# Kernel tuning notes

Measured on AMD Instinct MI355X. Metric: run time of the kernel, lower is better.

The kernel has to match this reference:

```python
import jax, jax.numpy as jnp
import numpy as np

HIDDEN = 1024
SENT = 1024
NS = 8192
NK = 8192


def setup_inputs() -> dict:
    key = jax.random.key(0)
    ks = jax.random.split(key, 6)
    scale = 0.02
    return {
        "sentences_embedding": jax.random.normal(ks[0], (NS, SENT), dtype=jnp.float32),
        "knowledge_embedding": jax.random.normal(ks[1], (NK, 2 * HIDDEN), dtype=jnp.float32),
        "Ws": jax.random.normal(ks[2], (HIDDEN, SENT), dtype=jnp.float32) * scale,
        "bs": jnp.zeros((HIDDEN,), dtype=jnp.float32),
        "Wk": jax.random.normal(ks[3], (HIDDEN, 2 * HIDDEN), dtype=jnp.float32) * scale,
        "bk": jnp.zeros((HIDDEN,), dtype=jnp.float32),
    }


def reference(sentences_embedding, knowledge_embedding, Ws, bs, Wk, bk):
    # S: [Ns, hidden], K: [Nk, hidden] (torch Linear: x @ W.T + b)
    S = sentences_embedding @ Ws.T + bs
    K = knowledge_embedding @ Wk.T + bk
    V = knowledge_embedding  # [Nk, 2*hidden]
    scores = S @ K.T  # [Ns, Nk]
    # NOTE: softmax over dim=0 (across sentences), per the original module
    attns = jax.nn.softmax(scores, axis=0)
    fused_knowledge = attns @ V  # [Ns, 2*hidden]
    return (attns, fused_knowledge)
```

## Files before the change

### kernel.cpp

```cpp
#include <hip/hip_runtime.h>
#include <hip/hip_bf16.h>
#include <math.h>

typedef __bf16 bf16_t;
typedef __bf16 bf16x8 __attribute__((ext_vector_type(8)));
typedef __bf16 bf16x4v __attribute__((ext_vector_type(4)));
typedef float floatx4 __attribute__((ext_vector_type(4)));

#define BM 128
#define BN 128
#define BK 64
#define BK2 128
#define LDT 72

__device__ __forceinline__ void gload_lds16(const void* g, void* l) {
    __builtin_amdgcn_global_load_lds(
        (__attribute__((address_space(1))) void*)g,
        (__attribute__((address_space(3))) void*)l,
        16, 0, 0);
}

__device__ __forceinline__ void split8(const float* p, bf16x8& hi, bf16x8& lo) {
    const float4* q = (const float4*)p;
    float4 a = q[0], b = q[1];
    float v[8] = { a.x, a.y, a.z, a.w, b.x, b.y, b.z, b.w };
#pragma unroll
    for (int i = 0; i < 8; ++i) {
        bf16_t h = (bf16_t)v[i];
        hi[i] = h;
        lo[i] = (bf16_t)(v[i] - (float)h);
    }
}

template<bool OUT_SPLIT, bool HAS_BIAS>
__global__ __launch_bounds__(256, 2)
void gemm_nt_split(const float* __restrict__ A, const float* __restrict__ B,
                   const float* __restrict__ bias,
                   void* __restrict__ C0, bf16_t* __restrict__ Clo,
                   int M, int N, int K)
{
    __shared__ bf16_t Ah[BM * LDT];
    __shared__ bf16_t Al[BM * LDT];
    __shared__ bf16_t Bh[BN * LDT];
    __shared__ bf16_t Bl[BN * LDT];

    const int t    = threadIdx.x;
    const int m0   = blockIdx.x * BM;
    const int n0   = blockIdx.y * BN;
    const int lane = t & 63;
    const int wm   = ((t >> 6) & 1) * 64;
    const int wn   = (t >> 7) * 64;
    const int lr   = lane & 15;
    const int lg   = lane >> 4;

    floatx4 acc[4][4] = {};

    for (int k0 = 0; k0 < K; k0 += BK) {
#pragma unroll
        for (int i = 0; i < 4; ++i) {
            int idx = t + i * 256;
            int row = idx >> 3;
            int col = (idx & 7) << 3;
            bf16x8 h, l;
            split8(&A[(size_t)(m0 + row) * K + k0 + col], h, l);
            *(bf16x8*)&Ah[row * LDT + col] = h;
            *(bf16x8*)&Al[row * LDT + col] = l;
            split8(&B[(size_t)(n0 + row) * K + k0 + col], h, l);
            *(bf16x8*)&Bh[row * LDT + col] = h;
            *(bf16x8*)&Bl[row * LDT + col] = l;
        }
        __syncthreads();
#pragma unroll
        for (int ks = 0; ks < BK; ks += 32) {
            bf16x8 ah[4], al[4], bh[4], bl[4];
#pragma unroll
            for (int mi = 0; mi < 4; ++mi) {
                ah[mi] = *(const bf16x8*)&Ah[(wm + mi * 16 + lr) * LDT + ks + lg * 8];
                al[mi] = *(const bf16x8*)&Al[(wm + mi * 16 + lr) * LDT + ks + lg * 8];
            }
#pragma unroll
            for (int ni = 0; ni < 4; ++ni) {
                bh[ni] = *(const bf16x8*)&Bh[(wn + ni * 16 + lr) * LDT + ks + lg * 8];
                bl[ni] = *(const bf16x8*)&Bl[(wn + ni * 16 + lr) * LDT + ks + lg * 8];
            }
#pragma unroll
            for (int mi = 0; mi < 4; ++mi)
#pragma unroll
                for (int ni = 0; ni < 4; ++ni) {
                    acc[mi][ni] = __builtin_amdgcn_mfma_f32_16x16x32_bf16(ah[mi], bh[ni], acc[mi][ni], 0, 0, 0);
                    acc[mi][ni] = __builtin_amdgcn_mfma_f32_16x16x32_bf16(ah[mi], bl[ni], acc[mi][ni], 0, 0, 0);
                    acc[mi][ni] = __builtin_amdgcn_mfma_f32_16x16x32_bf16(al[mi], bh[ni], acc[mi][ni], 0, 0, 0);
                }
        }
        __syncthreads();
    }

#pragma unroll
    for (int mi = 0; mi < 4; ++mi)
#pragma unroll
        for (int ni = 0; ni < 4; ++ni) {
            int col = n0 + wn + ni * 16 + lr;
            float bv = 0.0f;
            if constexpr (HAS_BIAS) bv = bias[col];
#pragma unroll
            for (int r = 0; r < 4; ++r) {
                int row = m0 + wm + mi * 16 + lg * 4 + r;
                float v = acc[mi][ni][r] + bv;
                if constexpr (OUT_SPLIT) {
                    bf16_t h = (bf16_t)v;
                    ((bf16_t*)C0)[(size_t)row * N + col] = h;
                    Clo[(size_t)row * N + col] = (bf16_t)(v - (float)h);
                } else {
                    ((float*)C0)[(size_t)row * N + col] = v;
                }
            }
        }
}

__global__ __launch_bounds__(256, 2)
void gemm_nt_pre_async(const bf16_t* __restrict__ Ahi, const bf16_t* __restrict__ Alo,
                       const bf16_t* __restrict__ Bhi, const bf16_t* __restrict__ Blo,
                       float* __restrict__ C, float* __restrict__ pm,
                       float* __restrict__ pz, int M, int N, int K)
{
    __shared__ bf16_t Ah[BM * BK];
    __shared__ bf16_t Al[BM * BK];
    __shared__ bf16_t Bh[BN * BK];
    __shared__ bf16_t Bl[BN * BK];
    __shared__ float red_m[2][128];
    __shared__ float red_z[2][128];

    const int t    = threadIdx.x;
    const int m0   = blockIdx.x * BM;
    const int n0   = blockIdx.y * BN;
    const int lane = t & 63;
    const int wv   = t >> 6;
    const int widm = (t >> 6) & 1;
    const int wm   = widm * 64;
    const int wn   = (t >> 7) * 64;
    const int lr   = lane & 15;
    const int lg   = lane >> 4;
    const int lrow = lane >> 3;
    const int lcol = (((lane & 7) ^ lrow) * 8);
    const int swz  = (lr & 7) << 3;

    floatx4 acc[4][4] = {};

    for (int k0 = 0; k0 < K; k0 += BK) {
#pragma unroll
        for (int i = 0; i < 4; ++i) {
            const int seg = wv * 4 + i;
            const int row = seg * 8 + lrow;
            const size_t ga = (size_t)(m0 + row) * K + k0 + lcol;
            const size_t gb = (size_t)(n0 + row) * K + k0 + lcol;
            gload_lds16(&Ahi[ga], &Ah[seg * 512]);
            gload_lds16(&Alo[ga], &Al[seg * 512]);
            gload_lds16(&Bhi[gb], &Bh[seg * 512]);
            gload_lds16(&Blo[gb], &Bl[seg * 512]);
        }
        __syncthreads();
#pragma unroll
        for (int ks = 0; ks < BK; ks += 32) {
            const int cA = (ks + lg * 8) ^ swz;
            bf16x8 ah[4], al[4], bh[4], bl[4];
#pragma unroll
            for (int mi = 0; mi < 4; ++mi) {
                ah[mi] = *(const bf16x8*)&Ah[(wm + mi * 16 + lr) * BK + cA];
                al[mi] = *(const bf16x8*)&Al[(wm + mi * 16 + lr) * BK + cA];
            }
#pragma unroll
            for (int ni = 0; ni < 4; ++ni) {
                bh[ni] = *(const bf16x8*)&Bh[(wn + ni * 16 + lr) * BK + cA];
                bl[ni] = *(const bf16x8*)&Bl[(wn + ni * 16 + lr) * BK + cA];
            }
#pragma unroll
            for (int mi = 0; mi < 4; ++mi)
#pragma unroll
                for (int ni = 0; ni < 4; ++ni) {
                    acc[mi][ni] = __builtin_amdgcn_mfma_f32_16x16x32_bf16(ah[mi], bh[ni], acc[mi][ni], 0, 0, 0);
                    acc[mi][ni] = __builtin_amdgcn_mfma_f32_16x16x32_bf16(ah[mi], bl[ni], acc[mi][ni], 0, 0, 0);
                    acc[mi][ni] = __builtin_amdgcn_mfma_f32_16x16x32_bf16(al[mi], bh[ni], acc[mi][ni], 0, 0, 0);
                }
        }
        __syncthreads();
    }

#pragma unroll
    for (int mi = 0; mi < 4; ++mi)
#pragma unroll
        for (int ni = 0; ni < 4; ++ni) {
            int col = n0 + wn + ni * 16 + lr;
#pragma unroll
            for (int r = 0; r < 4; ++r) {
                int row = m0 + wm + mi * 16 + lg * 4 + r;
                C[(size_t)row * N + col] = acc[mi][ni][r];
            }
        }

#pragma unroll
    for (int ni = 0; ni < 4; ++ni) {
        float lm = -INFINITY;
#pragma unroll
        for (int mi = 0; mi < 4; ++mi)
#pragma unroll
            for (int r = 0; r < 4; ++r) lm = fmaxf(lm, acc[mi][ni][r]);
        float lz = 0.0f;
#pragma unroll
        for (int mi = 0; mi < 4; ++mi)
#pragma unroll
            for (int r = 0; r < 4; ++r) lz += __expf(acc[mi][ni][r] - lm);
#pragma unroll
        for (int off = 16; off <= 32; off <<= 1) {
            float om = __shfl_xor(lm, off);
            float oz = __shfl_xor(lz, off);
            float nm = fmaxf(lm, om);
            lz = lz * __expf(lm - nm) + oz * __expf(om - nm);
            lm = nm;
        }
        if (lg == 0) {
            red_m[widm][wn + ni * 16 + lr] = lm;
            red_z[widm][wn + ni * 16 + lr] = lz;
        }
    }
    __syncthreads();
    if (t < 128) {
        float a = red_m[0][t], b = red_m[1][t];
        float za = red_z[0][t], zb = red_z[1][t];
        float mb = fmaxf(a, b);
        float z  = za * __expf(a - mb) + zb * __expf(b - mb);
        pm[(size_t)blockIdx.x * 8192 + n0 + t] = mb;
        pz[(size_t)blockIdx.x * 8192 + n0 + t] = z;
    }
}

__global__ __launch_bounds__(256, 2)
void gemm_nt_bf16_async(const bf16_t* __restrict__ A, const bf16_t* __restrict__ B,
                        float* __restrict__ C, int M, int N, int K)
{
    __shared__ bf16_t As[BM * BK2];
    __shared__ bf16_t Bs[BN * BK2];

    const int t    = threadIdx.x;
    const int m0   = blockIdx.x * BM;
    const int n0   = blockIdx.y * BN;
    const int lane = t & 63;
    const int wv   = t >> 6;
    const int wm   = ((t >> 6) & 1) * 64;
    const int wn   = (t >> 7) * 64;
    const int lr   = lane & 15;
    const int lg   = lane >> 4;
    const int srow = lane >> 4;
    const int sslt = lane & 15;
    const int swz  = (lr & 7) << 3;

    floatx4 acc[4][4] = {};

    for (int k0 = 0; k0 < K; k0 += BK2) {
#pragma unroll
        for (int i = 0; i < 8; ++i) {
            const int bi  = wv * 8 + i;
            const int row = bi * 4 + srow;
            const int gs  = (sslt & 8) | ((sslt & 7) ^ (row & 7));
            gload_lds16(&A[(size_t)(m0 + row) * K + k0 + gs * 8], &As[bi * 512]);
            gload_lds16(&B[(size_t)(n0 + row) * K + k0 + gs * 8], &Bs[bi * 512]);
        }
        __syncthreads();
#pragma unroll
        for (int ks = 0; ks < BK2; ks += 32) {
            const int cA = (ks + lg * 8) ^ swz;
            bf16x8 a[4], b[4];
#pragma unroll
            for (int mi = 0; mi < 4; ++mi)
                a[mi] = *(const bf16x8*)&As[(wm + mi * 16 + lr) * BK2 + cA];
#pragma unroll
            for (int ni = 0; ni < 4; ++ni)
                b[ni] = *(const bf16x8*)&Bs[(wn + ni * 16 + lr) * BK2 + cA];
#pragma unroll
            for (int mi = 0; mi < 4; ++mi)
#pragma unroll
                for (int ni = 0; ni < 4; ++ni)
                    acc[mi][ni] = __builtin_amdgcn_mfma_f32_16x16x32_bf16(
                        a[mi], b[ni], acc[mi][ni], 0, 0, 0);
        }
        __syncthreads();
    }

#pragma unroll
    for (int mi = 0; mi < 4; ++mi)
#pragma unroll
        for (int ni = 0; ni < 4; ++ni) {
            int col = n0 + wn + ni * 16 + lr;
#pragma unroll
            for (int r = 0; r < 4; ++r) {
                int row = m0 + wm + mi * 16 + lg * 4 + r;
                C[(size_t)row * N + col] = acc[mi][ni][r];
            }
        }
}

__global__ __launch_bounds__(256)
void transpose_to_bf16(const float* __restrict__ src, bf16_t* __restrict__ dst,
                       int R, int Ccols)
{
    __shared__ float tile[64][65];
    const int r0 = blockIdx.x * 64;
    const int c0 = blockIdx.y * 64;
    const int tr = threadIdx.x >> 4;
    const int tc = (threadIdx.x & 15) * 4;
#pragma unroll
    for (int i = 0; i < 4; ++i) {
        int r = tr + i * 16;
        float4 v = *(const float4*)&src[(size_t)(r0 + r) * Ccols + c0 + tc];
        tile[r][tc + 0] = v.x; tile[r][tc + 1] = v.y;
        tile[r][tc + 2] = v.z; tile[r][tc + 3] = v.w;
    }
    __syncthreads();
#pragma unroll
    for (int i = 0; i < 4; ++i) {
        int c = tr + i * 16;
        bf16x4v o = { (bf16_t)tile[tc + 0][c], (bf16_t)tile[tc + 1][c],
                      (bf16_t)tile[tc + 2][c], (bf16_t)tile[tc + 3][c] };
        *(bf16x4v*)&dst[(size_t)(c0 + c) * R + r0 + tc] = o;
    }
}

__global__ __launch_bounds__(256)
void col_softmax_combine64(const float* __restrict__ pm, const float* __restrict__ pz,
                           float* __restrict__ mf, float* __restrict__ iz)
{
    int j = blockIdx.x * 256 + threadIdx.x;
    float m = -INFINITY;
#pragma unroll
    for (int c = 0; c < 64; ++c) m = fmaxf(m, pm[(size_t)c * 8192 + j]);
    float z = 0.0f;
#pragma unroll
    for (int c = 0; c < 64; ++c) z += pz[(size_t)c * 8192 + j] * __expf(pm[(size_t)c * 8192 + j] - m);
    mf[j] = m;
    iz[j] = 1.0f / z;
}

__global__ __launch_bounds__(256)
void normalize_attn_bf16(float* __restrict__ sc, const float* __restrict__ mf,
                         const float* __restrict__ iz, bf16_t* __restrict__ ab)
{
    size_t base = ((size_t)blockIdx.x * 256 + threadIdx.x) * 4;
    int j = (int)(base & 8191);
    float4 s  = *(float4*)&sc[base];
    float4 m4 = *(const float4*)&mf[j];
    float4 z4 = *(const float4*)&iz[j];
    s.x = __expf(s.x - m4.x) * z4.x;
    s.y = __expf(s.y - m4.y) * z4.y;
    s.z = __expf(s.z - m4.z) * z4.z;
    s.w = __expf(s.w - m4.w) * z4.w;
    *(float4*)&sc[base] = s;
    bf16x4v b = { (bf16_t)s.x, (bf16_t)s.y, (bf16_t)s.z, (bf16_t)s.w };
    *(bf16x4v*)&ab[base] = b;
}

extern "C" void kernel_launch(void* const* d_in, const int* in_sizes, int n_in,
                              void* d_out, int out_size, void* d_ws, size_t ws_size,
                              hipStream_t stream) {
    const float* sent  = (const float*)d_in[0];
    const float* knowl = (const float*)d_in[1];
    const float* Ws    = (const float*)d_in[2];
    const float* bs    = (const float*)d_in[3];
    const float* Wk    = (const float*)d_in[4];
    const float* bk    = (const float*)d_in[5];

    float* attns = (float*)d_out;
    float* fused = (float*)d_out + (size_t)8192 * 8192;

    const size_t MB = 1024 * 1024;
    char* ws = (char*)d_ws;
    dim3 blk(256);

    bf16_t* Shi = (bf16_t*)(ws + 0 * MB);
    bf16_t* Slo = (bf16_t*)(ws + 16 * MB);
    bf16_t* Khi = (bf16_t*)(ws + 32 * MB);
    bf16_t* Klo = (bf16_t*)(ws + 48 * MB);
    bf16_t* Ab  = (bf16_t*)(ws);
    bf16_t* Vt  = (bf16_t*)(ws + 128 * MB);
    float*  pm  = (float*)(ws + 160 * MB);
    float*  pz  = (float*)(ws + 162 * MB);
    float*  mf  = (float*)(ws + 164 * MB);
    float*  iz  = mf + 8192;

    gemm_nt_split<true, true><<<dim3(64, 8), blk, 0, stream>>>(
        sent, Ws, bs, Shi, Slo, 8192, 1024, 1024);
    gemm_nt_split<true, true><<<dim3(64, 8), blk, 0, stream>>>(
        knowl, Wk, bk, Khi, Klo, 8192, 1024, 2048);
    gemm_nt_pre_async<<<dim3(64, 64), blk, 0, stream>>>(
        Shi, Slo, Khi, Klo, attns, pm, pz, 8192, 8192, 1024);
    transpose_to_bf16<<<dim3(128, 32), blk, 0, stream>>>(knowl, Vt, 8192, 2048);
    col_softmax_combine64<<<dim3(32), blk, 0, stream>>>(pm, pz, mf, iz);
    normalize_attn_bf16<<<dim3(65536), blk, 0, stream>>>(attns, mf, iz, Ab);
    gemm_nt_bf16_async<<<dim3(64, 16), blk, 0, stream>>>(
        Ab, Vt, fused, 8192, 2048, 8192);
}
```

Measured before the change: 1.335 ms.

## Add XCD-aware block swizzle to GEMMs and shrink final GEMM K tile

Remaps linear block IDs so that consecutive blocks scheduled onto the same XCD get contiguous tiles. This is meant to improve L2 reuse of shared A/B panels across the chiplets in all four GEMM kernels. The final attention-times-V GEMM also drops from a 128-wide K tile to a 64-wide one, using the XOR-swizzled LDS layout from the pre kernel. That halves LDS use per block but doubles the number of barrier iterations.

```diff
diff --git a/kernel.cpp b/kernel.cpp
--- a/kernel.cpp
+++ b/kernel.cpp
@@ -10,7 +10,6 @@
 #define BM 128
 #define BN 128
 #define BK 64
-#define BK2 128
 #define LDT 72
 
 __device__ __forceinline__ void gload_lds16(const void* g, void* l) {
@@ -20,6 +19,15 @@
         16, 0, 0);
 }
 
+__device__ __forceinline__ void xcd_swizzle(int gx, int gy, int& bx, int& by) {
+    const int nwg = gx * gy;
+    const int bid = (int)blockIdx.y * gx + (int)blockIdx.x;
+    const int cpx = nwg >> 3;
+    const int s   = (bid & 7) * cpx + (bid >> 3);
+    bx = s % gx;
+    by = s / gx;
+}
+
 __device__ __forceinline__ void split8(const float* p, bf16x8& hi, bf16x8& lo) {
     const float4* q = (const float4*)p;
     float4 a = q[0], b = q[1];
@@ -37,16 +45,19 @@
 void gemm_nt_split(const float* __restrict__ A, const float* __restrict__ B,
                    const float* __restrict__ bias,
                    void* __restrict__ C0, bf16_t* __restrict__ Clo,
-                   int M, int N, int K)
+                   int M, int N, int K, int gx, int gy)
 {
     __shared__ bf16_t Ah[BM * LDT];
     __shared__ bf16_t Al[BM * LDT];
     __shared__ bf16_t Bh[BN * LDT];
     __shared__ bf16_t Bl[BN * LDT];
 
+    int bx, by;
+    xcd_swizzle(gx, gy, bx, by);
+
     const int t    = threadIdx.x;
-    const int m0   = blockIdx.x * BM;
-    const int n0   = blockIdx.y * BN;
+    const int m0   = bx * BM;
+    const int n0   = by * BN;
     const int lane = t & 63;
     const int wm   = ((t >> 6) & 1) * 64;
     const int wn   = (t >> 7) * 64;
@@ -121,7 +132,7 @@
 void gemm_nt_pre_async(const bf16_t* __restrict__ Ahi, const bf16_t* __restrict__ Alo,
                        const bf16_t* __restrict__ Bhi, const bf16_t* __restrict__ Blo,
                        float* __restrict__ C, float* __restrict__ pm,
-                       float* __restrict__ pz, int M, int N, int K)
+                       float* __restrict__ pz, int M, int N, int K, int gx, int gy)
 {
     __shared__ bf16_t Ah[BM * BK];
     __shared__ bf16_t Al[BM * BK];
@@ -130,9 +141,12 @@
     __shared__ float red_m[2][128];
     __shared__ float red_z[2][128];
 
+    int bx, by;
+    xcd_swizzle(gx, gy, bx, by);
+
     const int t    = threadIdx.x;
-    const int m0   = blockIdx.x * BM;
-    const int n0   = blockIdx.y * BN;
+    const int m0   = bx * BM;
+    const int n0   = by * BN;
     const int lane = t & 63;
     const int wv   = t >> 6;
     const int widm = (t >> 6) & 1;
@@ -228,53 +242,55 @@
         float za = red_z[0][t], zb = red_z[1][t];
         float mb = fmaxf(a, b);
         float z  = za * __expf(a - mb) + zb * __expf(b - mb);
-        pm[(size_t)blockIdx.x * 8192 + n0 + t] = mb;
-        pz[(size_t)blockIdx.x * 8192 + n0 + t] = z;
+        pm[(size_t)bx * 8192 + n0 + t] = mb;
+        pz[(size_t)bx * 8192 + n0 + t] = z;
     }
 }
 
 __global__ __launch_bounds__(256, 2)
 void gemm_nt_bf16_async(const bf16_t* __restrict__ A, const bf16_t* __restrict__ B,
-                        float* __restrict__ C, int M, int N, int K)
-{
-    __shared__ bf16_t As[BM * BK2];
-    __shared__ bf16_t Bs[BN * BK2];
+                        float* __restrict__ C, int M, int N, int K, int gx, int gy)
+{
+    __shared__ bf16_t As[BM * BK];
+    __shared__ bf16_t Bs[BN * BK];
+
+    int bx, by;
+    xcd_swizzle(gx, gy, bx, by);
 
     const int t    = threadIdx.x;
-    const int m0   = blockIdx.x * BM;
-    const int n0   = blockIdx.y * BN;
+    const int m0   = bx * BM;
+    const int n0   = by * BN;
     const int lane = t & 63;
     const int wv   = t >> 6;
     const int wm   = ((t >> 6) & 1) * 64;
     const int wn   = (t >> 7) * 64;
     const int lr   = lane & 15;
     const int lg   = lane >> 4;
-    const int srow = lane >> 4;
-    const int sslt = lane & 15;
+    const int lrow = lane >> 3;
+    const int lcol = (((lane & 7) ^ lrow) * 8);
     const int swz  = (lr & 7) << 3;
 
     floatx4 acc[4][4] = {};
 
-    for (int k0 = 0; k0 < K; k0 += BK2) {
-#pragma unroll
-        for (int i = 0; i < 8; ++i) {
-            const int bi  = wv * 8 + i;
-            const int row = bi * 4 + srow;
-            const int gs  = (sslt & 8) | ((sslt & 7) ^ (row & 7));
-            gload_lds16(&A[(size_t)(m0 + row) * K + k0 + gs * 8], &As[bi * 512]);
-            gload_lds16(&B[(size_t)(n0 + row) * K + k0 + gs * 8], &Bs[bi * 512]);
-        }
-        __syncthreads();
-#pragma unroll
-        for (int ks = 0; ks < BK2; ks += 32) {
+    for (int k0 = 0; k0 < K; k0 += BK) {
+#pragma unroll
+        for (int i = 0; i < 4; ++i) {
+            const int seg = wv * 4 + i;
+            const int row = seg * 8 + lrow;
+            gload_lds16(&A[(size_t)(m0 + row) * K + k0 + lcol], &As[seg * 512]);
+            gload_lds16(&B[(size_t)(n0 + row) * K + k0 + lcol], &Bs[seg * 512]);
+        }
+        __syncthreads();
+#pragma unroll
+        for (int ks = 0; ks < BK; ks += 32) {
             const int cA = (ks + lg * 8) ^ swz;
             bf16x8 a[4], b[4];
 #pragma unroll
             for (int mi = 0; mi < 4; ++mi)
-                a[mi] = *(const bf16x8*)&As[(wm + mi * 16 + lr) * BK2 + cA];
+                a[mi] = *(const bf16x8*)&As[(wm + mi * 16 + lr) * BK + cA];
 #pragma unroll
             for (int ni = 0; ni < 4; ++ni)
-                b[ni] = *(const bf16x8*)&Bs[(wn + ni * 16 + lr) * BK2 + cA];
+                b[ni] = *(const bf16x8*)&Bs[(wn + ni * 16 + lr) * BK + cA];
 #pragma unroll
             for (int mi = 0; mi < 4; ++mi)
 #pragma unroll
@@ -386,14 +402,14 @@
     float*  iz  = mf + 8192;
 
     gemm_nt_split<true, true><<<dim3(64, 8), blk, 0, stream>>>(
-        sent, Ws, bs, Shi, Slo, 8192, 1024, 1024);
+        sent, Ws, bs, Shi, Slo, 8192, 1024, 1024, 64, 8);
     gemm_nt_split<true, true><<<dim3(64, 8), blk, 0, stream>>>(
-        knowl, Wk, bk, Khi, Klo, 8192, 1024, 2048);
+        knowl, Wk, bk, Khi, Klo, 8192, 1024, 2048, 64, 8);
     gemm_nt_pre_async<<<dim3(64, 64), blk, 0, stream>>>(
-        Shi, Slo, Khi, Klo, attns, pm, pz, 8192, 8192, 1024);
+        Shi, Slo, Khi, Klo, attns, pm, pz, 8192, 8192, 1024, 64, 64);
     transpose_to_bf16<<<dim3(128, 32), blk, 0, stream>>>(knowl, Vt, 8192, 2048);
     col_softmax_combine64<<<dim3(32), blk, 0, stream>>>(pm, pz, mf, iz);
     normalize_attn_bf16<<<dim3(65536), blk, 0, stream>>>(attns, mf, iz, Ab);
     gemm_nt_bf16_async<<<dim3(64, 16), blk, 0, stream>>>(
-        Ab, Vt, fused, 8192, 2048, 8192);
-}
+        Ab, Vt, fused, 8192, 2048, 8192, 64, 16);
+}
```

After: 1.367 ms. 1.02x slower.
